# Optimization experiments

Measured on AMD Instinct MI355X. Metric: run time of the kernel, lower is better.

Reference implementation:

```python
import jax, jax.numpy as jnp
import numpy as np
import math

B, Q_LEN, D, H, KV = 8, 2048, 1024, 16, 256
HD = D // H

def setup_inputs() -> dict:
    key0 = jax.random.key(0)
    ks = jax.random.split(key0, 6)
    query = jax.random.normal(ks[0], (B, Q_LEN, D), dtype=jnp.float32)
    key = jax.random.normal(ks[1], (B, 1024), dtype=jnp.float32)
    value = jax.random.normal(ks[2], (B, 1024), dtype=jnp.float32)
    clip_score = jax.random.uniform(ks[3], (B, KV), dtype=jnp.float32)
    # k_linear / v_linear weights (embed_dim, 1024), no bias
    k_weight = jax.random.normal(ks[4], (D, 1024), dtype=jnp.float32) * 0.02
    v_weight = jax.random.normal(ks[5], (D, 1024), dtype=jnp.float32) * 0.02
    # scale_linear: Linear(512, 1), weight const 0.05, bias const 7.5 (per nn.init.constant_)
    scale_w = jnp.full((2 * KV,), 0.05, dtype=jnp.float32)
    scale_b = jnp.array(7.5, dtype=jnp.float32)
    return {"query": query, "key": key, "value": value, "clip_score": clip_score,
            "k_weight": k_weight, "v_weight": v_weight, "scale_w": scale_w, "scale_b": scale_b}

def reference(query, key, value, clip_score, k_weight, v_weight, scale_w, scale_b):
    act_scale = 1.0
    b, qlen, d = query.shape
    # key/value are (B,1024): expand to (B,KV,1024) as in torch branch
    key_e = jnp.broadcast_to(key[:, None, :], (b, KV, key.shape[-1]))
    val_e = jnp.broadcast_to(value[:, None, :], (b, KV, value.shape[-1]))
    K = jnp.einsum('bkc,dc->bkd', key_e, k_weight)   # (B,KV,D)
    V = jnp.einsum('bkc,dc->bkd', val_e, v_weight)   # (B,KV,D)
    Qh = query.reshape(b, qlen, H, HD).transpose(0, 2, 1, 3)  # (B,H,Q,HD)
    Kh = K.reshape(b, KV, H, HD).transpose(0, 2, 1, 3)        # (B,H,KV,HD)
    Vh = V.reshape(b, KV, H, HD).transpose(0, 2, 1, 3)        # (B,H,KV,HD)
    scores = jnp.einsum('bhqd,bhkd->bhqk', Qh, Kh) / math.sqrt(HD)  # (B,H,Q,KV)
    # scale_linear(cat([scores, clip], -1)) == scores@w1 + clip@w2 + b (avoid materializing concat)
    w1, w2 = scale_w[:KV], scale_w[KV:]
    lin = (jnp.einsum('bhqk,k->bhq', scores, w1)[..., None]
           + (clip_score @ w2)[:, None, None, None] + scale_b)   # (B,H,Q,1)
    clip_e = clip_score[:, None, None, :]                        # (B,1,1,KV)
    scores = scores + (lin * clip_e) * act_scale
    attn_weights = jax.nn.softmax(scores, axis=-1)
    out = jnp.einsum('bhqk,bhkd->bhqd', attn_weights, Vh)
    out = out.transpose(0, 2, 1, 3).reshape(b, qlen, d)
    return (out, attn_weights)
```

## Files before the change

### kernel.cpp

```cpp
#include <hip/hip_runtime.h>
#include <hip/hip_bf16.h>

#define B_    8
#define QLEN  2048
#define D_    1024
#define H_    16
#define KV_   256
#define HD_   64

#define WS_KVEC 0
#define WS_VVEC 8192
#define WS_C2   16384
#define WS_SW1  16392

__device__ inline float wave_sum(float v) {
#pragma unroll
  for (int off = 32; off > 0; off >>= 1) v += __shfl_xor(v, off, 64);
  return v;
}
__device__ inline float wave_max(float v) {
#pragma unroll
  for (int off = 32; off > 0; off >>= 1) v = fmaxf(v, __shfl_xor(v, off, 64));
  return v;
}
__device__ inline float wave_min(float v) {
#pragma unroll
  for (int off = 32; off > 0; off >>= 1) v = fminf(v, __shfl_xor(v, off, 64));
  return v;
}

__global__ __launch_bounds__(256) void prep_kernel(
    const float* __restrict__ key, const float* __restrict__ value,
    const float* __restrict__ kw, const float* __restrict__ vw,
    const float* __restrict__ clip, const float* __restrict__ scale_w,
    float* __restrict__ ws) {
  const int lane = threadIdx.x & 63;
  const int waveId = threadIdx.x >> 6;

  if (blockIdx.x == 1024) {
    if (waveId != 0) return;
    const float4* sw4 = reinterpret_cast<const float4*>(scale_w);
    float4 a = sw4[lane];
    float s = wave_sum(a.x + a.y + a.z + a.w);
    if (lane == 0) ws[WS_SW1] = s;
    float4 w2 = sw4[64 + lane];
    for (int b = 0; b < B_; ++b) {
      const float4* c4 = reinterpret_cast<const float4*>(clip + b * KV_);
      float4 c = c4[lane];
      float p = c.x * w2.x + c.y * w2.y + c.z * w2.z + c.w * w2.w;
      p = wave_sum(p);
      if (lane == 0) ws[WS_C2 + b] = p;
    }
    return;
  }

  const int W = blockIdx.x * 4 + waveId;
  const int sel = W >> 11;
  const int rem = W & 2047;
  const int b = rem >> 8;
  const int g = rem & 255;
  const float* x = (sel ? value : key) + b * 1024;
  const float* Wt = sel ? vw : kw;
  const float4* x4 = reinterpret_cast<const float4*>(x);
  float4 xs[4];
#pragma unroll
  for (int i = 0; i < 4; ++i) xs[i] = x4[i * 64 + lane];
  float* outv = ws + (sel ? WS_VVEC : WS_KVEC) + b * 1024;
#pragma unroll
  for (int r = 0; r < 4; ++r) {
    const int d = g * 4 + r;
    const float4* w4 = reinterpret_cast<const float4*>(Wt + (size_t)d * 1024);
    float acc = 0.f;
#pragma unroll
    for (int i = 0; i < 4; ++i) {
      float4 w = w4[i * 64 + lane];
      acc += xs[i].x * w.x + xs[i].y * w.y + xs[i].z * w.z + xs[i].w * w.w;
    }
    acc = wave_sum(acc);
    if (lane == 0) outv[d] = acc;
  }
}

__global__ __launch_bounds__(256) void attn_kernel(
    const float* __restrict__ query, const float* __restrict__ clip,
    const float* __restrict__ scale_b, const float* __restrict__ ws,
    float* __restrict__ attn) {
  const int lane = threadIdx.x & 63;
  const int waveId = threadIdx.x >> 6;
  const int rowBase = blockIdx.x * 64 + waveId * 16;
  const int b = rowBase >> 15;
  const int h = (rowBase >> 11) & 15;
  const int q0 = rowBase & 2047;

  const float kv = ws[WS_KVEC + b * 1024 + h * 64 + lane];
  const float4* c4 = reinterpret_cast<const float4*>(clip + b * KV_);
  const float4 cl = c4[lane];
  const float cmax = wave_max(fmaxf(fmaxf(cl.x, cl.y), fmaxf(cl.z, cl.w)));
  const float cmin = wave_min(fminf(fminf(cl.x, cl.y), fminf(cl.z, cl.w)));
  const float sw1 = ws[WS_SW1];
  const float Lc = ws[WS_C2 + b] + scale_b[0];

  const float* qbase = query + ((size_t)(b * QLEN + q0)) * D_ + h * HD_ + lane;
  float qv[16];
#pragma unroll
  for (int r = 0; r < 16; ++r) qv[r] = qbase[(size_t)r * D_];

  float4* a4 = reinterpret_cast<float4*>(attn) + (size_t)rowBase * 64 + lane;
#pragma unroll
  for (int r = 0; r < 16; ++r) {
    const float s = wave_sum(qv[r] * kv);
    const float L = sw1 * (s * 0.125f) + Lc;
    const float m = (L >= 0.f) ? L * cmax : L * cmin;
    float4 e;
    e.x = __expf(L * cl.x - m);
    e.y = __expf(L * cl.y - m);
    e.z = __expf(L * cl.z - m);
    e.w = __expf(L * cl.w - m);
    const float den = wave_sum(e.x + e.y + e.z + e.w);
    const float rd = 1.0f / den;
    e.x *= rd; e.y *= rd; e.z *= rd; e.w *= rd;
    a4[(size_t)r * 64] = e;
  }
}

__global__ __launch_bounds__(256) void out_kernel(const float* __restrict__ ws,
                                                  float* __restrict__ out) {
  const float4* v4 = reinterpret_cast<const float4*>(ws + WS_VVEC);
  float4* o4 = reinterpret_cast<float4*>(out);
  const int idx = blockIdx.x * 256 + threadIdx.x;
#pragma unroll
  for (int i = 0; i < 4; ++i) {
    const int j = idx + i * 1048576;
    const int b = j >> 19;
    const int d4 = j & 255;
    o4[j] = v4[b * 256 + d4];
  }
}

extern "C" void kernel_launch(void* const* d_in, const int* in_sizes, int n_in,
                              void* d_out, int out_size, void* d_ws, size_t ws_size,
                              hipStream_t stream) {
  const float* query   = (const float*)d_in[0];
  const float* key     = (const float*)d_in[1];
  const float* value   = (const float*)d_in[2];
  const float* clip    = (const float*)d_in[3];
  const float* kw      = (const float*)d_in[4];
  const float* vw      = (const float*)d_in[5];
  const float* scale_w = (const float*)d_in[6];
  const float* scale_b = (const float*)d_in[7];
  float* out  = (float*)d_out;
  float* attn = out + (size_t)B_ * QLEN * D_;
  float* ws   = (float*)d_ws;

  hipLaunchKernelGGL(prep_kernel, dim3(1025), dim3(256), 0, stream,
                     key, value, kw, vw, clip, scale_w, ws);
  hipLaunchKernelGGL(attn_kernel, dim3(4096), dim3(256), 0, stream,
                     query, clip, scale_b, ws, attn);
  hipLaunchKernelGGL(out_kernel, dim3(4096), dim3(256), 0, stream, ws, out);
}
```

Before: 96.87 us.

## Fuse output broadcast into attention kernel, pair reductions, use nontemporal memory ops

Folds the output-broadcast kernel into the attention kernel, so one launch writes both the attention weights and the broadcast V rows. The per-row wave reductions now handle two rows at once through a paired shuffle that shares the xor-32 step. Query loads and all large stores become nontemporal to avoid polluting the cache on streaming traffic. This removes one kernel launch and its tail, at the cost of a longer attention kernel that mixes two store streams.

```diff
diff --git a/kernel.cpp b/kernel.cpp
--- a/kernel.cpp
+++ b/kernel.cpp
@@ -7,6 +7,8 @@
 #define H_    16
 #define KV_   256
 #define HD_   64
+
+typedef float fvec4 __attribute__((ext_vector_type(4)));
 
 #define WS_KVEC 0
 #define WS_VVEC 8192
@@ -27,6 +29,18 @@
 #pragma unroll
   for (int off = 32; off > 0; off >>= 1) v = fminf(v, __shfl_xor(v, off, 64));
   return v;
+}
+
+__device__ inline void pair_sum(float p0, float p1, int lane, float& s0, float& s1) {
+  const bool lo = (lane < 32);
+  float x = lo ? p1 : p0;
+  float t = __shfl_xor(x, 32, 64);
+  float c = (lo ? p0 : p1) + t;
+#pragma unroll
+  for (int off = 16; off > 0; off >>= 1) c += __shfl_xor(c, off, 64);
+  float u = __shfl_xor(c, 32, 64);
+  s0 = lo ? c : u;
+  s1 = lo ? u : c;
 }
 
 __global__ __launch_bounds__(256) void prep_kernel(
@@ -84,7 +98,7 @@
 __global__ __launch_bounds__(256) void attn_kernel(
     const float* __restrict__ query, const float* __restrict__ clip,
     const float* __restrict__ scale_b, const float* __restrict__ ws,
-    float* __restrict__ attn) {
+    float* __restrict__ attn, float* __restrict__ out) {
   const int lane = threadIdx.x & 63;
   const int waveId = threadIdx.x >> 6;
   const int rowBase = blockIdx.x * 64 + waveId * 16;
@@ -103,37 +117,44 @@
   const float* qbase = query + ((size_t)(b * QLEN + q0)) * D_ + h * HD_ + lane;
   float qv[16];
 #pragma unroll
-  for (int r = 0; r < 16; ++r) qv[r] = qbase[(size_t)r * D_];
+  for (int r = 0; r < 16; ++r) qv[r] = __builtin_nontemporal_load(&qbase[(size_t)r * D_]);
 
-  float4* a4 = reinterpret_cast<float4*>(attn) + (size_t)rowBase * 64 + lane;
+  fvec4* a4 = reinterpret_cast<fvec4*>(attn) + (size_t)rowBase * 64 + lane;
 #pragma unroll
-  for (int r = 0; r < 16; ++r) {
-    const float s = wave_sum(qv[r] * kv);
-    const float L = sw1 * (s * 0.125f) + Lc;
-    const float m = (L >= 0.f) ? L * cmax : L * cmin;
-    float4 e;
-    e.x = __expf(L * cl.x - m);
-    e.y = __expf(L * cl.y - m);
-    e.z = __expf(L * cl.z - m);
-    e.w = __expf(L * cl.w - m);
-    const float den = wave_sum(e.x + e.y + e.z + e.w);
-    const float rd = 1.0f / den;
-    e.x *= rd; e.y *= rd; e.z *= rd; e.w *= rd;
-    a4[(size_t)r * 64] = e;
+  for (int r = 0; r < 16; r += 2) {
+    float s0, s1;
+    pair_sum(qv[r] * kv, qv[r + 1] * kv, lane, s0, s1);
+    const float L0 = sw1 * (s0 * 0.125f) + Lc;
+    const float L1 = sw1 * (s1 * 0.125f) + Lc;
+    const float m0 = (L0 >= 0.f) ? L0 * cmax : L0 * cmin;
+    const float m1 = (L1 >= 0.f) ? L1 * cmax : L1 * cmin;
+    fvec4 e0, e1;
+    e0.x = __expf(L0 * cl.x - m0); e0.y = __expf(L0 * cl.y - m0);
+    e0.z = __expf(L0 * cl.z - m0); e0.w = __expf(L0 * cl.w - m0);
+    e1.x = __expf(L1 * cl.x - m1); e1.y = __expf(L1 * cl.y - m1);
+    e1.z = __expf(L1 * cl.z - m1); e1.w = __expf(L1 * cl.w - m1);
+    float den0, den1;
+    pair_sum(e0.x + e0.y + e0.z + e0.w, e1.x + e1.y + e1.z + e1.w, lane, den0, den1);
+    const float rd0 = 1.0f / den0;
+    const float rd1 = 1.0f / den1;
+    e0 *= rd0;
+    e1 *= rd1;
+    __builtin_nontemporal_store(e0, &a4[(size_t)r * 64]);
+    __builtin_nontemporal_store(e1, &a4[(size_t)(r + 1) * 64]);
   }
-}
 
-__global__ __launch_bounds__(256) void out_kernel(const float* __restrict__ ws,
-                                                  float* __restrict__ out) {
-  const float4* v4 = reinterpret_cast<const float4*>(ws + WS_VVEC);
-  float4* o4 = reinterpret_cast<float4*>(out);
-  const int idx = blockIdx.x * 256 + threadIdx.x;
+  {
+    const fvec4* v4 = reinterpret_cast<const fvec4*>(ws + WS_VVEC);
+    fvec4* o4 = reinterpret_cast<fvec4*>(out);
+    const int idx = blockIdx.x * 256 + threadIdx.x;
 #pragma unroll
-  for (int i = 0; i < 4; ++i) {
-    const int j = idx + i * 1048576;
-    const int b = j >> 19;
-    const int d4 = j & 255;
-    o4[j] = v4[b * 256 + d4];
+    for (int i = 0; i < 4; ++i) {
+      const int j = idx + i * 1048576;
+      const int ob = j >> 19;
+      const int d4 = j & 255;
+      fvec4 v = v4[ob * 256 + d4];
+      __builtin_nontemporal_store(v, &o4[j]);
+    }
   }
 }
 
@@ -155,6 +176,5 @@
   hipLaunchKernelGGL(prep_kernel, dim3(1025), dim3(256), 0, stream,
                      key, value, kw, vw, clip, scale_w, ws);
   hipLaunchKernelGGL(attn_kernel, dim3(4096), dim3(256), 0, stream,
-                     query, clip, scale_b, ws, attn);
-  hipLaunchKernelGGL(out_kernel, dim3(4096), dim3(256), 0, stream, ws, out);
+                     query, clip, scale_b, ws, attn, out);
 }
```

New measurement: 88.08 us. 1.1x faster.
